# Optimization experiments

Measured on AMD Instinct MI355X. Metric: run time of the kernel, lower is better.

## Reference

```python
import jax, jax.numpy as jnp
import numpy as np

B, S, D = 2, 2048, 1024
H, Dh = 16, 64  # qkv_features=1024, head_dim=64
F = 1024        # out_features


def setup_inputs() -> dict:
    key = jax.random.key(0)
    ks = jax.random.split(key, 16)
    s = 0.02
    return {
        'inputs_q': jax.random.normal(ks[0], (B, S, D), jnp.float32),
        'inputs_kv': jax.random.normal(ks[1], (B, S, D), jnp.float32),
        'pos_embed': jax.random.normal(ks[2], (S, D), jnp.float32),
        'Wq': jax.random.normal(ks[3], (D, H, Dh), jnp.float32) * s,
        'bq': jnp.zeros((H, Dh), jnp.float32),
        'Wk': jax.random.normal(ks[4], (D, H, Dh), jnp.float32) * s,
        'bk': jnp.zeros((H, Dh), jnp.float32),
        'Wv': jax.random.normal(ks[5], (D, H, Dh), jnp.float32) * s,
        'bv': jnp.zeros((H, Dh), jnp.float32),
        'Wpos': jax.random.normal(ks[6], (D, H, Dh), jnp.float32) * s,
        'r_r_bias': jax.random.normal(ks[7], (H, Dh), jnp.float32) * s,
        'r_w_bias': jax.random.normal(ks[8], (H, Dh), jnp.float32) * s,
        'Wout': jax.random.normal(ks[9], (H, Dh, F), jnp.float32) * s,
        'bout': jnp.zeros((F,), jnp.float32),
    }


_roll_vmap = jax.vmap(jnp.roll, in_axes=(-2, 0, None), out_axes=-2)


def reference(inputs_q, inputs_kv, pos_embed, Wq, bq, Wk, bk, Wv, bv,
              Wpos, r_r_bias, r_w_bias, Wout, bout):
    # QKV projections: [B,S,D] x [D,H,Dh] -> [B,S,H,Dh]
    q = jnp.einsum('bsd,dhk->bshk', inputs_q, Wq) + bq
    k = jnp.einsum('bsd,dhk->bshk', inputs_kv, Wk) + bk
    v = jnp.einsum('bsd,dhk->bshk', inputs_kv, Wv) + bv
    # relative position embedding projection: [S,D] -> [S,H,Dh]
    r_pos = jnp.einsum('sd,dhk->shk', pos_embed, Wpos)

    q_len = q.shape[-3]
    depth = q.shape[-1]
    # content score + relative-position score, both [B,H,S,S]
    aw = jnp.einsum('bqhd,bkhd->bhqk', q + r_w_bias, k)
    aw_r = jnp.einsum('bqhd,khd->bhqk', q + r_r_bias, r_pos)
    # Transformer-XL relative shift: per query-row roll along key axis
    shifts = jnp.arange(0, q_len) - (q_len - 1)
    aw_r = _roll_vmap(aw_r, shifts, -1)
    aw = (aw + aw_r) / jnp.sqrt(depth).astype(aw.dtype)
    attn = jax.nn.softmax(aw, axis=-1)
    # weighted sum: [B,S,H,Dh]
    x = jnp.einsum('bhqk,bkhd->bqhd', attn, v)
    # output projection contracting (H,Dh)
    out = jnp.einsum('bqhd,hdf->bqf', x, Wout) + bout
    return out
```

## Files before the change

kernel.cpp:

```cpp
#include <hip/hip_runtime.h>
#include <hip/hip_bf16.h>
#include <hip/hip_fp16.h>


#define B_  2
#define S_  2048
#define D_  1024
#define H_  16
#define DH_ 64
#define HD_ 1024
#define F_  1024
#define N_  4096
#define KC_ 512
#define SP2 520

typedef __attribute__((ext_vector_type(8))) short  short8;
typedef __attribute__((ext_vector_type(4))) float  floatx4;

__device__ __forceinline__ unsigned short f2bf(float x) {
  unsigned u = __float_as_uint(x);
  u += 0x7FFFu + ((u >> 16) & 1u);
  return (unsigned short)(u >> 16);
}
__device__ __forceinline__ unsigned short f2h(float x) {
  __half h = __float2half(x);
  unsigned short u; __builtin_memcpy(&u, &h, 2);
  return u;
}
__device__ __forceinline__ float h2f(unsigned short u) {
  __half h; __builtin_memcpy(&h, &u, 2);
  return __half2float(h);
}

#define CQ_ (N_ * D_ / 4)
__global__ void cast_all(const float* __restrict__ sq, const float* __restrict__ skv,
                         const float* __restrict__ spos,
                         unsigned short* __restrict__ dq, unsigned short* __restrict__ dkv,
                         unsigned short* __restrict__ dpos) {
  int i = blockIdx.x * blockDim.x + threadIdx.x;
  const float* s; unsigned short* d; int off;
  if (i < CQ_)            { s = sq;   d = dq;   off = i; }
  else if (i < 2 * CQ_)   { s = skv;  d = dkv;  off = i - CQ_; }
  else                    { s = spos; d = dpos; off = i - 2 * CQ_; }
  float4 v = ((const float4*)s)[off];
  ushort4 o = make_ushort4(f2bf(v.x), f2bf(v.y), f2bf(v.z), f2bf(v.w));
  ((ushort4*)d)[off] = o;
}

struct TP5 { const float* s[5]; unsigned short* d[5]; };
__global__ void transpose_all(TP5 p) {
  __shared__ float t[32][33];
  const float* src = p.s[blockIdx.z];
  unsigned short* dst = p.d[blockIdx.z];
  int c0 = blockIdx.x * 32, r0 = blockIdx.y * 32;
  int tx = threadIdx.x, ty = threadIdx.y;
#pragma unroll
  for (int i = 0; i < 4; i++)
    t[ty + i * 8][tx] = src[(size_t)(r0 + ty + i * 8) * 1024 + c0 + tx];
  __syncthreads();
#pragma unroll
  for (int i = 0; i < 4; i++)
    dst[(size_t)(c0 + ty + i * 8) * 1024 + r0 + tx] = f2bf(t[tx][ty + i * 8]);
}

__launch_bounds__(256, 2)
__global__ void gemm_bt(const unsigned short* A, const unsigned short* Bt,
                        const float* bias, const float* b2a, const float* b2b,
                        unsigned short* outA, unsigned short* outB, float* outF,
                        int Nn, int K, int mode, int split,
                        const unsigned short* A2, const unsigned short* Bt2,
                        const float* bias2, unsigned short* outA2, int mode2) {
  __shared__ unsigned short As[128 * 64];
  __shared__ unsigned short Bs[128 * 64];
  int bx = blockIdx.x;
  if (split && bx >= split) {
    bx -= split; A = A2; Bt = Bt2; bias = bias2; outA = outA2; mode = mode2;
    b2a = nullptr; b2b = nullptr;
  }
  int nb = Nn >> 7;
  int bm = bx / nb, bn = bx % nb;
  int tid = threadIdx.x;
  int lane = tid & 63, wv = tid >> 6;
  int wm = wv >> 1, wn = wv & 1;
  int lm = lane & 15, lg = lane >> 4;
  const unsigned short* Ab = A + (size_t)(bm * 128) * K;
  const unsigned short* Bb = Bt + (size_t)(bn * 128) * K;
  floatx4 acc[4][4];
#pragma unroll
  for (int i = 0; i < 4; i++)
#pragma unroll
    for (int j = 0; j < 4; j++) acc[i][j] = (floatx4){0.f, 0.f, 0.f, 0.f};

  int lr = tid >> 3;
  int lc = (tid & 7) * 8;
  for (int k0 = 0; k0 < K; k0 += 64) {
    __syncthreads();
#pragma unroll
    for (int i = 0; i < 4; i++) {
      int r = i * 32 + lr;
      *(uint4*)&As[r * 64 + lc] = *(const uint4*)&Ab[(size_t)r * K + k0 + lc];
      *(uint4*)&Bs[r * 64 + lc] = *(const uint4*)&Bb[(size_t)r * K + k0 + lc];
    }
    __syncthreads();
#pragma unroll
    for (int kk = 0; kk < 2; kk++) {
      short8 af[4], bf[4];
#pragma unroll
      for (int i = 0; i < 4; i++)
        af[i] = *(const short8*)&As[(wm * 64 + i * 16 + lm) * 64 + kk * 32 + lg * 8];
#pragma unroll
      for (int j = 0; j < 4; j++)
        bf[j] = *(const short8*)&Bs[(wn * 64 + j * 16 + lm) * 64 + kk * 32 + lg * 8];
#pragma unroll
      for (int i = 0; i < 4; i++)
#pragma unroll
        for (int j = 0; j < 4; j++)
          acc[i][j] = __builtin_amdgcn_mfma_f32_16x16x32_bf16(af[i], bf[j], acc[i][j], 0, 0, 0);
    }
  }
#pragma unroll
  for (int j = 0; j < 4; j++) {
    int col = bn * 128 + wn * 64 + j * 16 + lm;
    float bs = bias ? bias[col] : 0.f;
    float ba = b2a ? b2a[col] : 0.f;
    float bb = b2b ? b2b[col] : 0.f;
#pragma unroll
    for (int i = 0; i < 4; i++) {
      int row0 = bm * 128 + wm * 64 + i * 16 + lg * 4;
      if (mode == 4) {
        int s = row0 & 2047, bb2 = row0 >> 11;
        size_t vidx = (((size_t)bb2 * H_ + (col >> 6)) * 64 + (col & 63)) * (size_t)S_ + s;
        ushort4 o = make_ushort4(f2bf(acc[i][j][0] + bs), f2bf(acc[i][j][1] + bs),
                                 f2bf(acc[i][j][2] + bs), f2bf(acc[i][j][3] + bs));
        *(ushort4*)&outA[vidx] = o;
      } else {
#pragma unroll
        for (int r = 0; r < 4; r++) {
          float v = acc[i][j][r] + bs;
          size_t idx = (size_t)(row0 + r) * Nn + col;
          if (mode == 0)      outA[idx] = f2bf(v);
          else if (mode == 1) { outA[idx] = f2bf(v + ba); outB[idx] = f2bf(v + bb); }
          else                outF[idx] = v;
        }
      }
    }
  }
}

__launch_bounds__(512, 4)
__global__ void attn_kernel(const unsigned short* __restrict__ qw,
                            const unsigned short* __restrict__ qr,
                            const unsigned short* __restrict__ kb,
                            const unsigned short* __restrict__ rb,
                            const unsigned short* __restrict__ vt,
                            unsigned short* __restrict__ xb) {
  __shared__ __align__(16) unsigned short sS[2][32 * SP2];
  __shared__ float sSum[8][32];
  __shared__ float sLinv[32];
  int bid = blockIdx.x;
  int qt = bid & 63;
  int bh = bid >> 6;
  int b = bh >> 4, h = bh & 15;
  int q0 = qt * 32;
  int tid = threadIdx.x;
  int lane = tid & 63, wv = tid >> 6;
  int lm = lane & 15, lg = lane >> 4;

  short8 bqw[2][2], bqr[2][2];
  const size_t qbase = (size_t)(b * S_ + q0) * HD_ + h * 64;
#pragma unroll
  for (int t = 0; t < 2; t++) {
    const unsigned short* p1 = qw + qbase + (size_t)(t * 16 + lm) * HD_ + lg * 8;
    const unsigned short* p2 = qr + qbase + (size_t)(t * 16 + lm) * HD_ + lg * 8;
    bqw[t][0] = *(const short8*)(p1);
    bqw[t][1] = *(const short8*)(p1 + 32);
    bqr[t][0] = *(const short8*)(p2);
    bqr[t][1] = *(const short8*)(p2 + 32);
  }

  floatx4 acc[2][4];
#pragma unroll
  for (int m = 0; m < 2; m++)
#pragma unroll
    for (int j = 0; j < 4; j++) acc[m][j] = (floatx4){0.f, 0.f, 0.f, 0.f};
  float s0 = 0.f, s1 = 0.f;

  const unsigned short* vb0 = vt + (size_t)(b * H_ + h) * 64 * S_;
  const float KSC = 0.1803368801111204f;

  for (int c = 0; c < 4; c++) {
    unsigned short* S = sS[c & 1];
    int kc = c * KC_;
    for (int jt = wv; jt < 34; jt += 8) {
      int jrow = (kc - q0 - 32 + jt * 16 + lm) & 2047;
      const unsigned short* rp = rb + (size_t)jrow * HD_ + h * 64 + lg * 8;
      short8 a0 = *(const short8*)(rp);
      short8 a1 = *(const short8*)(rp + 32);
#pragma unroll
      for (int t = 0; t < 2; t++) {
        floatx4 c4 = (floatx4){0.f, 0.f, 0.f, 0.f};
        c4 = __builtin_amdgcn_mfma_f32_16x16x32_bf16(a0, bqr[t][0], c4, 0, 0, 0);
        c4 = __builtin_amdgcn_mfma_f32_16x16x32_bf16(a1, bqr[t][1], c4, 0, 0, 0);
        int q = t * 16 + lm;
        int ub = jt * 16 + lg * 4 + q - 31;
        unsigned short* row = &S[q * SP2];
#pragma unroll
        for (int r = 0; r < 4; r++) {
          int u = ub + r;
          if ((unsigned)u < (unsigned)KC_) row[u] = f2h(c4[r]);
        }
      }
    }
    __syncthreads();
#pragma unroll 2
    for (int kt = 0; kt < 4; kt++) {
      int u0 = wv * 64 + kt * 16;
      const unsigned short* kp = kb + (size_t)(b * S_ + kc + u0 + lm) * HD_ + h * 64 + lg * 8;
      short8 a0 = *(const short8*)(kp);
      short8 a1 = *(const short8*)(kp + 32);
#pragma unroll
      for (int t = 0; t < 2; t++) {
        floatx4 c4 = (floatx4){0.f, 0.f, 0.f, 0.f};
        c4 = __builtin_amdgcn_mfma_f32_16x16x32_bf16(a0, bqw[t][0], c4, 0, 0, 0);
        c4 = __builtin_amdgcn_mfma_f32_16x16x32_bf16(a1, bqw[t][1], c4, 0, 0, 0);
        int q = t * 16 + lm;
        ushort4* p = (ushort4*)&S[q * SP2 + u0 + lg * 4];
        ushort4 Rv = *p;
        float p0 = exp2f((c4[0] + h2f(Rv.x)) * KSC);
        float p1 = exp2f((c4[1] + h2f(Rv.y)) * KSC);
        float p2 = exp2f((c4[2] + h2f(Rv.z)) * KSC);
        float p3 = exp2f((c4[3] + h2f(Rv.w)) * KSC);
        float ps = (p0 + p1) + (p2 + p3);
        if (t == 0) s0 += ps; else s1 += ps;
        *p = make_ushort4(f2bf(p0), f2bf(p1), f2bf(p2), f2bf(p3));
      }
    }
    __syncthreads();
#pragma unroll
    for (int s = 0; s < 2; s++) {
      int u0 = wv * 64 + s * 32;
      short8 a0 = *(short8*)&S[lm * SP2 + u0 + lg * 8];
      short8 a1 = *(short8*)&S[(16 + lm) * SP2 + u0 + lg * 8];
      const unsigned short* vp = vb0 + kc + u0 + lg * 8;
#pragma unroll
      for (int j = 0; j < 4; j++) {
        short8 bb = *(const short8*)&vp[(size_t)(j * 16 + lm) * S_];
        acc[0][j] = __builtin_amdgcn_mfma_f32_16x16x32_bf16(a0, bb, acc[0][j], 0, 0, 0);
        acc[1][j] = __builtin_amdgcn_mfma_f32_16x16x32_bf16(a1, bb, acc[1][j], 0, 0, 0);
      }
    }
  }
  s0 += __shfl_xor(s0, 16); s0 += __shfl_xor(s0, 32);
  s1 += __shfl_xor(s1, 16); s1 += __shfl_xor(s1, 32);
  if (lane < 16) { sSum[wv][lane] = s0; sSum[wv][16 + lane] = s1; }
  __syncthreads();
  if (tid < 32) {
    float t = 0.f;
#pragma unroll
    for (int w = 0; w < 8; w++) t += sSum[w][tid];
    sLinv[tid] = 1.f / t;
  }
  float* po = (float*)sS;
#pragma unroll
  for (int m = 0; m < 2; m++)
#pragma unroll
    for (int j = 0; j < 4; j++)
#pragma unroll
      for (int r = 0; r < 4; r++) {
        int q = m * 16 + lg * 4 + r;
        int dh = j * 16 + lm;
        po[wv * 2048 + q * 64 + dh] = acc[m][j][r];
      }
  __syncthreads();
  {
    int e = tid * 4;
    int q = e >> 6, dh = e & 63;
    float4 v = *(float4*)&po[e];
#pragma unroll
    for (int w = 1; w < 8; w++) {
      float4 u = *(float4*)&po[w * 2048 + e];
      v.x += u.x; v.y += u.y; v.z += u.z; v.w += u.w;
    }
    float li = sLinv[q];
    ushort4 o = make_ushort4(f2bf(v.x * li), f2bf(v.y * li), f2bf(v.z * li), f2bf(v.w * li));
    *(ushort4*)&xb[(size_t)(b * S_ + q0 + q) * HD_ + h * 64 + dh] = o;
  }
}

extern "C" void kernel_launch(void* const* d_in, const int* in_sizes, int n_in,
                              void* d_out, int out_size, void* d_ws, size_t ws_size,
                              hipStream_t stream) {
  const float* inputs_q  = (const float*)d_in[0];
  const float* inputs_kv = (const float*)d_in[1];
  const float* pos_embed = (const float*)d_in[2];
  const float* Wq   = (const float*)d_in[3];
  const float* bq   = (const float*)d_in[4];
  const float* Wk   = (const float*)d_in[5];
  const float* bk   = (const float*)d_in[6];
  const float* Wv   = (const float*)d_in[7];
  const float* bv   = (const float*)d_in[8];
  const float* Wpos = (const float*)d_in[9];
  const float* rrb  = (const float*)d_in[10];
  const float* rwb  = (const float*)d_in[11];
  const float* Wout = (const float*)d_in[12];
  const float* bout = (const float*)d_in[13];
  float* out = (float*)d_out;

  char* ws = (char*)d_ws;
  unsigned short* aq  = (unsigned short*)(ws);
  unsigned short* akv = (unsigned short*)(ws + ( 8u << 20));
  unsigned short* apo = (unsigned short*)(ws + (16u << 20));
  unsigned short* wqt = (unsigned short*)(ws + (20u << 20));
  unsigned short* wkt = (unsigned short*)(ws + (22u << 20));
  unsigned short* wvt = (unsigned short*)(ws + (24u << 20));
  unsigned short* wpt = (unsigned short*)(ws + (26u << 20));
  unsigned short* wot = (unsigned short*)(ws + (28u << 20));
  unsigned short* qwp = (unsigned short*)(ws + (30u << 20));
  unsigned short* qrp = (unsigned short*)(ws + (38u << 20));
  unsigned short* kbp = (unsigned short*)(ws + (46u << 20));
  unsigned short* vtp = (unsigned short*)(ws + (54u << 20));
  unsigned short* rbp = (unsigned short*)(ws + (62u << 20));
  unsigned short* xbp = aq;

  cast_all<<<10240, 256, 0, stream>>>(inputs_q, inputs_kv, pos_embed, aq, akv, apo);
  TP5 tp;
  tp.s[0] = Wq; tp.s[1] = Wk; tp.s[2] = Wv; tp.s[3] = Wpos; tp.s[4] = Wout;
  tp.d[0] = wqt; tp.d[1] = wkt; tp.d[2] = wvt; tp.d[3] = wpt; tp.d[4] = wot;
  transpose_all<<<dim3(32, 32, 5), dim3(32, 8), 0, stream>>>(tp);

  gemm_bt<<<256 + 128, 256, 0, stream>>>(aq, wqt, bq, rwb, rrb, qwp, qrp, nullptr,
                                         HD_, D_, 1, 256, apo, wpt, nullptr, rbp, 0);
  gemm_bt<<<512, 256, 0, stream>>>(akv, wkt, bk, nullptr, nullptr, kbp, nullptr, nullptr,
                                   HD_, D_, 0, 256, akv, wvt, bv, vtp, 4);
  attn_kernel<<<2048, 512, 0, stream>>>(qwp, qrp, kbp, rbp, vtp, xbp);
  gemm_bt<<<256, 256, 0, stream>>>(xbp, wot, bout, nullptr, nullptr, nullptr, nullptr, out,
                                   F_, HD_, 2, 0, nullptr, nullptr, nullptr, nullptr, 0);
}
```

Before: 433.0 us.

## Halve attention LDS, fold softmax scale into Q, use direct global-to-LDS loads

The attention kernel drops its double-buffered score tile for a single buffer plus an extra barrier per chunk. It also reduces the final cross-wave accumulator in two halves so the smaller LDS suffices, and raises the launch-bounds occupancy hint to 8. The softmax scale is folded into the q-with-bias projections in the GEMM epilogue, and probabilities use a cheaper round-half-up bf16 conversion. GEMM tile staging switches to global_load_lds direct loads. The trade-off is more barriers and tighter register limits, plus slightly different rounding.

Result: slower. 698.1 us (+61.2%).

```diff
diff --git a/kernel.cpp b/kernel.cpp
--- a/kernel.cpp
+++ b/kernel.cpp
@@ -22,6 +22,9 @@
   u += 0x7FFFu + ((u >> 16) & 1u);
   return (unsigned short)(u >> 16);
 }
+__device__ __forceinline__ unsigned short f2bf_rhu(float x) {
+  return (unsigned short)((__float_as_uint(x) + 0x8000u) >> 16);
+}
 __device__ __forceinline__ unsigned short f2h(float x) {
   __half h = __float2half(x);
   unsigned short u; __builtin_memcpy(&u, &h, 2);
@@ -30,6 +33,10 @@
 __device__ __forceinline__ float h2f(unsigned short u) {
   __half h; __builtin_memcpy(&h, &u, 2);
   return __half2float(h);
+}
+__device__ __forceinline__ void gld_lds16(const unsigned short* g, unsigned short* l) {
+  __builtin_amdgcn_global_load_lds((const __attribute__((address_space(1))) void*)g,
+                                   (__attribute__((address_space(3))) void*)l, 16, 0, 0);
 }
 
 #define CQ_ (N_ * D_ / 4)
@@ -98,8 +105,8 @@
 #pragma unroll
     for (int i = 0; i < 4; i++) {
       int r = i * 32 + lr;
-      *(uint4*)&As[r * 64 + lc] = *(const uint4*)&Ab[(size_t)r * K + k0 + lc];
-      *(uint4*)&Bs[r * 64 + lc] = *(const uint4*)&Bb[(size_t)r * K + k0 + lc];
+      gld_lds16(&Ab[(size_t)r * K + k0 + lc], &As[r * 64 + lc]);
+      gld_lds16(&Bb[(size_t)r * K + k0 + lc], &Bs[r * 64 + lc]);
     }
     __syncthreads();
 #pragma unroll
@@ -118,6 +125,7 @@
           acc[i][j] = __builtin_amdgcn_mfma_f32_16x16x32_bf16(af[i], bf[j], acc[i][j], 0, 0, 0);
     }
   }
+  const float KSC = 0.1803368801111204f;
 #pragma unroll
   for (int j = 0; j < 4; j++) {
     int col = bn * 128 + wn * 64 + j * 16 + lm;
@@ -139,7 +147,7 @@
           float v = acc[i][j][r] + bs;
           size_t idx = (size_t)(row0 + r) * Nn + col;
           if (mode == 0)      outA[idx] = f2bf(v);
-          else if (mode == 1) { outA[idx] = f2bf(v + ba); outB[idx] = f2bf(v + bb); }
+          else if (mode == 1) { outA[idx] = f2bf((v + ba) * KSC); outB[idx] = f2bf((v + bb) * KSC); }
           else                outF[idx] = v;
         }
       }
@@ -147,14 +155,14 @@
   }
 }
 
-__launch_bounds__(512, 4)
+__launch_bounds__(512, 8)
 __global__ void attn_kernel(const unsigned short* __restrict__ qw,
                             const unsigned short* __restrict__ qr,
                             const unsigned short* __restrict__ kb,
                             const unsigned short* __restrict__ rb,
                             const unsigned short* __restrict__ vt,
                             unsigned short* __restrict__ xb) {
-  __shared__ __align__(16) unsigned short sS[2][32 * SP2];
+  __shared__ __align__(16) unsigned short sS[32 * SP2];
   __shared__ float sSum[8][32];
   __shared__ float sLinv[32];
   int bid = blockIdx.x;
@@ -186,10 +194,8 @@
   float s0 = 0.f, s1 = 0.f;
 
   const unsigned short* vb0 = vt + (size_t)(b * H_ + h) * 64 * S_;
-  const float KSC = 0.1803368801111204f;
 
   for (int c = 0; c < 4; c++) {
-    unsigned short* S = sS[c & 1];
     int kc = c * KC_;
     for (int jt = wv; jt < 34; jt += 8) {
       int jrow = (kc - q0 - 32 + jt * 16 + lm) & 2047;
@@ -203,7 +209,7 @@
         c4 = __builtin_amdgcn_mfma_f32_16x16x32_bf16(a1, bqr[t][1], c4, 0, 0, 0);
         int q = t * 16 + lm;
         int ub = jt * 16 + lg * 4 + q - 31;
-        unsigned short* row = &S[q * SP2];
+        unsigned short* row = &sS[q * SP2];
 #pragma unroll
         for (int r = 0; r < 4; r++) {
           int u = ub + r;
@@ -224,23 +230,23 @@
         c4 = __builtin_amdgcn_mfma_f32_16x16x32_bf16(a0, bqw[t][0], c4, 0, 0, 0);
         c4 = __builtin_amdgcn_mfma_f32_16x16x32_bf16(a1, bqw[t][1], c4, 0, 0, 0);
         int q = t * 16 + lm;
-        ushort4* p = (ushort4*)&S[q * SP2 + u0 + lg * 4];
+        ushort4* p = (ushort4*)&sS[q * SP2 + u0 + lg * 4];
         ushort4 Rv = *p;
-        float p0 = exp2f((c4[0] + h2f(Rv.x)) * KSC);
-        float p1 = exp2f((c4[1] + h2f(Rv.y)) * KSC);
-        float p2 = exp2f((c4[2] + h2f(Rv.z)) * KSC);
-        float p3 = exp2f((c4[3] + h2f(Rv.w)) * KSC);
+        float p0 = exp2f(c4[0] + h2f(Rv.x));
+        float p1 = exp2f(c4[1] + h2f(Rv.y));
+        float p2 = exp2f(c4[2] + h2f(Rv.z));
+        float p3 = exp2f(c4[3] + h2f(Rv.w));
         float ps = (p0 + p1) + (p2 + p3);
         if (t == 0) s0 += ps; else s1 += ps;
-        *p = make_ushort4(f2bf(p0), f2bf(p1), f2bf(p2), f2bf(p3));
+        *p = make_ushort4(f2bf_rhu(p0), f2bf_rhu(p1), f2bf_rhu(p2), f2bf_rhu(p3));
       }
     }
     __syncthreads();
 #pragma unroll
     for (int s = 0; s < 2; s++) {
       int u0 = wv * 64 + s * 32;
-      short8 a0 = *(short8*)&S[lm * SP2 + u0 + lg * 8];
-      short8 a1 = *(short8*)&S[(16 + lm) * SP2 + u0 + lg * 8];
+      short8 a0 = *(short8*)&sS[lm * SP2 + u0 + lg * 8];
+      short8 a1 = *(short8*)&sS[(16 + lm) * SP2 + u0 + lg * 8];
       const unsigned short* vp = vb0 + kc + u0 + lg * 8;
 #pragma unroll
       for (int j = 0; j < 4; j++) {
@@ -249,10 +255,24 @@
         acc[1][j] = __builtin_amdgcn_mfma_f32_16x16x32_bf16(a1, bb, acc[1][j], 0, 0, 0);
       }
     }
+    __syncthreads();
   }
   s0 += __shfl_xor(s0, 16); s0 += __shfl_xor(s0, 32);
   s1 += __shfl_xor(s1, 16); s1 += __shfl_xor(s1, 32);
   if (lane < 16) { sSum[wv][lane] = s0; sSum[wv][16 + lane] = s1; }
+  float* po = (float*)sS;
+  if (wv >= 4) {
+#pragma unroll
+    for (int m = 0; m < 2; m++)
+#pragma unroll
+      for (int j = 0; j < 4; j++)
+#pragma unroll
+        for (int r = 0; r < 4; r++) {
+          int q = m * 16 + lg * 4 + r;
+          int dh = j * 16 + lm;
+          po[(wv - 4) * 2048 + q * 64 + dh] = acc[m][j][r];
+        }
+  }
   __syncthreads();
   if (tid < 32) {
     float t = 0.f;
@@ -260,24 +280,25 @@
     for (int w = 0; w < 8; w++) t += sSum[w][tid];
     sLinv[tid] = 1.f / t;
   }
-  float* po = (float*)sS;
-#pragma unroll
-  for (int m = 0; m < 2; m++)
-#pragma unroll
-    for (int j = 0; j < 4; j++)
-#pragma unroll
-      for (int r = 0; r < 4; r++) {
-        int q = m * 16 + lg * 4 + r;
-        int dh = j * 16 + lm;
-        po[wv * 2048 + q * 64 + dh] = acc[m][j][r];
-      }
+  if (wv < 4) {
+#pragma unroll
+    for (int m = 0; m < 2; m++)
+#pragma unroll
+      for (int j = 0; j < 4; j++)
+#pragma unroll
+        for (int r = 0; r < 4; r++) {
+          int q = m * 16 + lg * 4 + r;
+          int dh = j * 16 + lm;
+          po[wv * 2048 + q * 64 + dh] += acc[m][j][r];
+        }
+  }
   __syncthreads();
   {
     int e = tid * 4;
     int q = e >> 6, dh = e & 63;
     float4 v = *(float4*)&po[e];
 #pragma unroll
-    for (int w = 1; w < 8; w++) {
+    for (int w = 1; w < 4; w++) {
       float4 u = *(float4*)&po[w * 2048 + e];
       v.x += u.x; v.y += u.y; v.z += u.z; v.w += u.w;
     }
```
